# Kernel tuning notes

Measured on AMD Instinct MI355X. Metric: run time of the kernel, lower is better.

The kernel has to match this reference:

```python
import jax, jax.numpy as jnp
import numpy as np

D_MODEL = 1024
NUM_HEADS = 16
HEAD_DIM = D_MODEL // NUM_HEADS


def setup_inputs() -> dict:
    key = jax.random.key(0)
    ks = jax.random.split(key, 11)
    B, S, D = 2, 2048, D_MODEL
    s = 1.0 / np.sqrt(D)
    return {
        "query": jax.random.normal(ks[0], (B, S, D), jnp.float32),
        "key": jax.random.normal(ks[1], (B, S, D), jnp.float32),
        "value": jax.random.normal(ks[2], (B, S, D), jnp.float32),
        "w_q": jax.random.normal(ks[3], (D, D), jnp.float32) * s,
        "b_q": jnp.zeros((D,), jnp.float32),
        "w_k": jax.random.normal(ks[4], (D, D), jnp.float32) * s,
        "b_k": jnp.zeros((D,), jnp.float32),
        "w_v": jax.random.normal(ks[5], (D, D), jnp.float32) * s,
        "b_v": jnp.zeros((D,), jnp.float32),
        "w_o": jax.random.normal(ks[6], (D, D), jnp.float32) * s,
        "b_o": jnp.zeros((D,), jnp.float32),
    }


def reference(query, key, value, w_q, b_q, w_k, b_k, w_v, b_v, w_o, b_o):
    B, S, D = query.shape
    H, Hd = NUM_HEADS, HEAD_DIM
    # Linear layers (torch convention: x @ W.T + b)
    Q = (query @ w_q.T + b_q).reshape(B, S, H, Hd).transpose(0, 2, 1, 3)  # [B,H,S,Hd]
    K = (key @ w_k.T + b_k).reshape(B, S, H, Hd).transpose(0, 2, 1, 3)
    V = (value @ w_v.T + b_v).reshape(B, S, H, Hd).transpose(0, 2, 1, 3)
    scale = jnp.float32(np.sqrt(Hd))
    scores = jnp.einsum("bhqd,bhkd->bhqk", Q, K) / scale  # [B,H,S,S]
    attn_weights = jax.nn.softmax(scores, axis=-1)
    # dropout is identity in eval mode
    out = jnp.einsum("bhqk,bhkd->bhqd", attn_weights, V)  # [B,H,S,Hd]
    out = out.transpose(0, 2, 1, 3).reshape(B, S, D)
    out = out @ w_o.T + b_o
    return out, attn_weights
```

## Files before the change

kernel.cpp:

```cpp
#include <hip/hip_runtime.h>
#include <hip/hip_bf16.h>
#include <stdint.h>
#include <math.h>

typedef __attribute__((ext_vector_type(8))) short bf16x8;
typedef __attribute__((ext_vector_type(4))) float f32x4;
typedef __attribute__((ext_vector_type(8))) unsigned short ushort8;
typedef __attribute__((ext_vector_type(4))) unsigned short ushort4v;

#define LDS_AS(p) ((__attribute__((address_space(3))) void*)(p))
#define GLB_AS(p) ((const __attribute__((address_space(1))) void*)(p))

#define EXP2F(x) __builtin_amdgcn_exp2f(x)

__device__ __forceinline__ unsigned short f2bf(float f) {
  uint32_t u = __builtin_bit_cast(uint32_t, f);
  u += 0x7FFFu + ((u >> 16) & 1u);
  return (unsigned short)(u >> 16);
}

__global__ __launch_bounds__(256) void cvt_all_kernel(
    const float* __restrict__ q, const float* __restrict__ k, const float* __restrict__ v,
    const float* __restrict__ wq, const float* __restrict__ wk,
    const float* __restrict__ wv, const float* __restrict__ wo,
    unsigned short* __restrict__ oq, unsigned short* __restrict__ ok, unsigned short* __restrict__ ov,
    unsigned short* __restrict__ owq, unsigned short* __restrict__ owk,
    unsigned short* __restrict__ owv, unsigned short* __restrict__ owo) {
  int i = blockIdx.x * 256 + threadIdx.x;
  const float* src; unsigned short* dst; int off;
  if (i < 1572864) {
    int tsel = i / 524288; off = i - tsel * 524288;
    src = (tsel == 0) ? q : (tsel == 1) ? k : v;
    dst = (tsel == 0) ? oq : (tsel == 1) ? ok : ov;
  } else {
    int j = i - 1572864; int tsel = j >> 17; off = j & 131071;
    src = (tsel == 0) ? wq : (tsel == 1) ? wk : (tsel == 2) ? wv : wo;
    dst = (tsel == 0) ? owq : (tsel == 1) ? owk : (tsel == 2) ? owv : owo;
  }
  const f32x4* p = (const f32x4*)src + (size_t)off * 2;
  f32x4 a = p[0], b = p[1];
  ushort8 r;
  r[0] = f2bf(a[0]); r[1] = f2bf(a[1]); r[2] = f2bf(a[2]); r[3] = f2bf(a[3]);
  r[4] = f2bf(b[0]); r[5] = f2bf(b[1]); r[6] = f2bf(b[2]); r[7] = f2bf(b[3]);
  *((ushort8*)dst + off) = r;
}

template <int MODE>
__device__ __forceinline__ void gemm_bt_body(const unsigned short* __restrict__ A,
                                             const unsigned short* __restrict__ W,
                                             const float* __restrict__ bias,
                                             void* __restrict__ Cout, int N, int K,
                                             int mtile, int ntile) {
  __shared__ unsigned short As[128 * 64];
  __shared__ unsigned short Bs[128 * 64];
  const int t = threadIdx.x;
  const int lane = t & 63, wid = t >> 6;
  const int grp = lane >> 4, lr = lane & 15;
  const int wm = wid >> 1, wn = wid & 1;
  f32x4 acc[4][4] = {};
  for (int kt = 0; kt < K; kt += 64) {
    __syncthreads();
#pragma unroll
    for (int i = 0; i < 4; ++i) {
      int off = (i * 256 + t) * 16;
      int row = off >> 7, u8 = (off >> 4) & 7;
      const unsigned short* sa = A + (size_t)(mtile + row) * K + kt + u8 * 8;
      __builtin_amdgcn_global_load_lds(GLB_AS(sa), LDS_AS((char*)As + off), 16, 0, 0);
      const unsigned short* sb = W + (size_t)(ntile + row) * K + kt + u8 * 8;
      __builtin_amdgcn_global_load_lds(GLB_AS(sb), LDS_AS((char*)Bs + off), 16, 0, 0);
    }
    __syncthreads();
#pragma unroll
    for (int kc = 0; kc < 2; ++kc) {
      bf16x8 af[4], bfr[4];
#pragma unroll
      for (int mf = 0; mf < 4; ++mf) {
        int row = wm * 64 + mf * 16 + lr;
        af[mf] = *(const bf16x8*)((const char*)As + row * 128 + kc * 64 + grp * 16);
      }
#pragma unroll
      for (int nf = 0; nf < 4; ++nf) {
        int row = wn * 64 + nf * 16 + lr;
        bfr[nf] = *(const bf16x8*)((const char*)Bs + row * 128 + kc * 64 + grp * 16);
      }
#pragma unroll
      for (int mf = 0; mf < 4; ++mf)
#pragma unroll
        for (int nf = 0; nf < 4; ++nf)
          acc[mf][nf] = __builtin_amdgcn_mfma_f32_16x16x32_bf16(af[mf], bfr[nf], acc[mf][nf], 0, 0, 0);
    }
  }
#pragma unroll
  for (int nf = 0; nf < 4; ++nf) {
    int gcol = ntile + wn * 64 + nf * 16 + lr;
    float bv = bias[gcol];
#pragma unroll
    for (int mf = 0; mf < 4; ++mf) {
      int grow0 = mtile + wm * 64 + mf * 16 + grp * 4;
      if (MODE == 2) {
        ushort4v cv;
#pragma unroll
        for (int j = 0; j < 4; ++j) cv[j] = f2bf(acc[mf][nf][j] + bv);
        int bh = ((grow0 >> 11) << 4) | (gcol >> 6);
        *(ushort4v*)((unsigned short*)Cout +
                     ((size_t)(bh * 64 + (gcol & 63))) * 2048 + (grow0 & 2047)) = cv;
      } else {
#pragma unroll
        for (int j = 0; j < 4; ++j) {
          float v = acc[mf][nf][j] + bv;
          if (MODE == 1) ((unsigned short*)Cout)[(size_t)(grow0 + j) * N + gcol] = f2bf(v);
          else           ((float*)Cout)[(size_t)(grow0 + j) * N + gcol] = v;
        }
      }
    }
  }
}

__device__ __forceinline__ void gemm_swz(int& mtile, int& ntile) {
  int d0 = blockIdx.y * 8 + blockIdx.x;
  int L = (d0 & 7) * 32 + (d0 >> 3);
  ntile = (L & 7) * 128;
  mtile = (L >> 3) * 128;
}

__global__ __launch_bounds__(256) void gemm_qkv_kernel(
    const unsigned short* Xq, const unsigned short* Xk, const unsigned short* Xv,
    const unsigned short* Wq, const unsigned short* Wk, const unsigned short* Wv,
    const float* bq, const float* bk, const float* bv,
    unsigned short* Cq, unsigned short* Ck, unsigned short* Vt) {
  int mtile, ntile; gemm_swz(mtile, ntile);
  int z = blockIdx.z;
  if (z == 2)      gemm_bt_body<2>(Xv, Wv, bv, Vt, 1024, 1024, mtile, ntile);
  else if (z == 1) gemm_bt_body<1>(Xk, Wk, bk, Ck, 1024, 1024, mtile, ntile);
  else             gemm_bt_body<1>(Xq, Wq, bq, Cq, 1024, 1024, mtile, ntile);
}

__global__ __launch_bounds__(256) void gemm_out_kernel(const unsigned short* ctx,
                                                       const unsigned short* Wo,
                                                       const float* bo, float* out) {
  int mtile, ntile; gemm_swz(mtile, ntile);
  gemm_bt_body<0>(ctx, Wo, bo, out, 1024, 1024, mtile, ntile);
}

__global__ __launch_bounds__(256) void attn_kernel(const unsigned short* __restrict__ Qb,
                                                   const unsigned short* __restrict__ Kb,
                                                   const unsigned short* __restrict__ Vt,
                                                   float* __restrict__ attn,
                                                   unsigned short* __restrict__ ctx) {
  __shared__ unsigned short QP[4096];
  __shared__ unsigned short Ks[2][4096];
  __shared__ unsigned short Vs[2][4096];
  const int t = threadIdx.x;
  const int lane = t & 63, wid = t >> 6;
  const int grp = lane >> 4, lr = lane & 15;
  const int d0 = blockIdx.y * 32 + blockIdx.x;
  const int L = (d0 & 7) * 128 + (d0 >> 3);
  const int bh = L >> 5, qt = L & 31;
  const int b = bh >> 4, h = bh & 15;
  const int qbase = qt * 64;
  const unsigned short* Qg = Qb + ((size_t)(b * 2048 + qbase) * 1024 + h * 64);
  const unsigned short* Kg = Kb + ((size_t)(b * 2048) * 1024 + h * 64);
  const unsigned short* Vg = Vt + (size_t)bh * 64 * 2048;

  auto stageK = [&](int kt, int bs) {
#pragma unroll
    for (int i = 0; i < 2; ++i) {
      int off = (i * 256 + t) * 16;
      int row = off >> 7, u = (off >> 4) & 7, us = u ^ (row & 7);
      __builtin_amdgcn_global_load_lds(
          GLB_AS((const char*)(Kg + (size_t)kt * 64 * 1024) + row * 2048 + us * 16),
          LDS_AS((char*)Ks[bs] + off), 16, 0, 0);
    }
  };
  auto stageV = [&](int kt, int bs) {
#pragma unroll
    for (int i = 0; i < 2; ++i) {
      int off = (i * 256 + t) * 16;
      int row = off >> 7, u = (off >> 4) & 7, us = u ^ (row & 7);
      __builtin_amdgcn_global_load_lds(
          GLB_AS((const char*)(Vg + kt * 64) + row * 4096 + us * 16),
          LDS_AS((char*)Vs[bs] + off), 16, 0, 0);
    }
  };

#pragma unroll
  for (int i = 0; i < 2; ++i) {
    int off = (i * 256 + t) * 16;
    int row = off >> 7, u = (off >> 4) & 7, us = u ^ (row & 7);
    __builtin_amdgcn_global_load_lds(GLB_AS((const char*)Qg + row * 2048 + us * 16),
                                     LDS_AS((char*)QP + off), 16, 0, 0);
  }
  stageK(0, 0);
  __syncthreads();
  bf16x8 qf[2];
#pragma unroll
  for (int kc = 0; kc < 2; ++kc) {
    int row = wid * 16 + lr, c2 = kc * 64 + grp * 16;
    qf[kc] = *(const bf16x8*)((const char*)QP + (((row << 7) | c2) ^ ((row & 7) << 4)));
  }

  const float C1 = 0.18033688011112042f;
  float lsum = 0.f;
  for (int kt = 0; kt < 32; ++kt) {
    if (kt < 31) stageK(kt + 1, (kt + 1) & 1);
    const char* Kc = (const char*)Ks[kt & 1];
    f32x4 sacc[4] = {};
#pragma unroll
    for (int kc = 0; kc < 2; ++kc)
#pragma unroll
      for (int mf = 0; mf < 4; ++mf) {
        int row = mf * 16 + lr, c2 = kc * 64 + grp * 16;
        bf16x8 kf = *(const bf16x8*)(Kc + (((row << 7) | c2) ^ ((row & 7) << 4)));
        sacc[mf] = __builtin_amdgcn_mfma_f32_16x16x32_bf16(kf, qf[kc], sacc[mf], 0, 0, 0);
      }
#pragma unroll
    for (int mf = 0; mf < 4; ++mf)
#pragma unroll
      for (int j = 0; j < 4; ++j)
        lsum += EXP2F(sacc[mf][j] * C1);
    __syncthreads();
  }
  lsum += __shfl_xor(lsum, 16);
  lsum += __shfl_xor(lsum, 32);
  const float nl2l = -log2f(lsum);

  f32x4 oacc[4] = {};
  unsigned short* Pw = &QP[wid * 1024];
  const int q4 = lane >> 4, kseg = lane & 15;
  float* abase = attn + ((size_t)bh * 2048 + qbase + wid * 16) * 2048 + kseg * 4;
  stageK(0, 0); stageV(0, 0);
  __syncthreads();
  for (int kt = 0; kt < 32; ++kt) {
    if (kt < 31) { stageK(kt + 1, (kt + 1) & 1); stageV(kt + 1, (kt + 1) & 1); }
    __builtin_amdgcn_sched_barrier(0);
    const int cur = kt & 1;
    const char* Kc = (const char*)Ks[cur];
    const char* Vc = (const char*)Vs[cur];
    f32x4 sacc[4] = {};
#pragma unroll
    for (int kc = 0; kc < 2; ++kc)
#pragma unroll
      for (int mf = 0; mf < 4; ++mf) {
        int row = mf * 16 + lr, c2 = kc * 64 + grp * 16;
        bf16x8 kf = *(const bf16x8*)(Kc + (((row << 7) | c2) ^ ((row & 7) << 4)));
        sacc[mf] = __builtin_amdgcn_mfma_f32_16x16x32_bf16(kf, qf[kc], sacc[mf], 0, 0, 0);
      }
#pragma unroll
    for (int mf = 0; mf < 4; ++mf) {
      f32x4 pv;
#pragma unroll
      for (int j = 0; j < 4; ++j) pv[j] = EXP2F(__builtin_fmaf(sacc[mf][j], C1, nl2l));
      ushort4v pb;
#pragma unroll
      for (int j = 0; j < 4; ++j) pb[j] = f2bf(pv[j]);
      int c2 = (mf * 16 + grp * 4) * 2;
      *(ushort4v*)((char*)Pw + (((lr << 7) | c2) ^ ((lr & 7) << 4))) = pb;
    }
#pragma unroll
    for (int kc = 0; kc < 2; ++kc) {
      int c2 = kc * 64 + grp * 16;
      bf16x8 pf = *(const bf16x8*)((const char*)Pw + (((lr << 7) | c2) ^ ((lr & 7) << 4)));
#pragma unroll
      for (int df = 0; df < 4; ++df) {
        int row = df * 16 + lr;
        bf16x8 vf = *(const bf16x8*)(Vc + (((row << 7) | c2) ^ ((row & 7) << 4)));
        oacc[df] = __builtin_amdgcn_mfma_f32_16x16x32_bf16(vf, pf, oacc[df], 0, 0, 0);
      }
    }
#pragma unroll
    for (int i = 0; i < 4; ++i) {
      int qrow = i * 4 + q4;
      ushort4v pb4 = *(const ushort4v*)((const char*)Pw +
                       (((qrow << 7) | (kseg * 8)) ^ ((qrow & 7) << 4)));
      f32x4 pf4;
#pragma unroll
      for (int j = 0; j < 4; ++j)
        pf4[j] = __builtin_bit_cast(float, (uint32_t)((uint32_t)(unsigned short)pb4[j] << 16));
      __builtin_nontemporal_store(pf4, (f32x4*)(abase + (size_t)qrow * 2048 + kt * 64));
    }
    asm volatile("s_waitcnt vmcnt(4) lgkmcnt(0)" ::: "memory");
    __builtin_amdgcn_sched_barrier(0);
    __builtin_amdgcn_s_barrier();
  }
  unsigned short* crow = ctx + ((size_t)(b * 2048 + qbase + wid * 16 + lr) * 1024 + h * 64);
#pragma unroll
  for (int df = 0; df < 4; ++df) {
    ushort4v cv;
#pragma unroll
    for (int j = 0; j < 4; ++j) cv[j] = f2bf(oacc[df][j]);
    *(ushort4v*)(crow + df * 16 + grp * 4) = cv;
  }
}

extern "C" void kernel_launch(void* const* d_in, const int* in_sizes, int n_in,
                              void* d_out, int out_size, void* d_ws, size_t ws_size,
                              hipStream_t stream) {
  const float* query = (const float*)d_in[0];
  const float* key   = (const float*)d_in[1];
  const float* value = (const float*)d_in[2];
  const float* w_q = (const float*)d_in[3];
  const float* b_q = (const float*)d_in[4];
  const float* w_k = (const float*)d_in[5];
  const float* b_k = (const float*)d_in[6];
  const float* w_v = (const float*)d_in[7];
  const float* b_v = (const float*)d_in[8];
  const float* w_o = (const float*)d_in[9];
  const float* b_o = (const float*)d_in[10];

  float* out  = (float*)d_out;
  float* attn = out + (size_t)2 * 2048 * 1024;

  unsigned short* ws = (unsigned short*)d_ws;
  unsigned short* Xq = ws;
  unsigned short* Xk = Xq + 4194304;
  unsigned short* Xv = Xk + 4194304;
  unsigned short* Wq = Xv + 4194304;
  unsigned short* Wk = Wq + 1048576;
  unsigned short* Wv = Wk + 1048576;
  unsigned short* Wo = Wv + 1048576;
  unsigned short* Qb = Wo + 1048576;
  unsigned short* Kb = Qb + 4194304;
  unsigned short* Vt = Kb + 4194304;
  unsigned short* ctx = Vt + 4194304;

  cvt_all_kernel<<<8192, 256, 0, stream>>>(query, key, value, w_q, w_k, w_v, w_o,
                                           Xq, Xk, Xv, Wq, Wk, Wv, Wo);
  gemm_qkv_kernel<<<dim3(8, 32, 3), 256, 0, stream>>>(Xq, Xk, Xv, Wq, Wk, Wv,
                                                      b_q, b_k, b_v, Qb, Kb, Vt);
  attn_kernel<<<dim3(32, 32), 256, 0, stream>>>(Qb, Kb, Vt, attn, ctx);
  gemm_out_kernel<<<dim3(8, 32), 256, 0, stream>>>(ctx, Wo, b_o, out);
}
```

Before: 232.6 us.

## Split attention into separate row-sum and PV kernels via global lse buffer

Moves the first pass, which computes softmax row sums without subtracting a max, out of the fused attention kernel into its own lightweight kernel that writes -log2(sum) per query row to a workspace buffer. The second kernel reads that value, stages the first K/V tiles earlier, and only does the probability write-out and PV pass. The smaller kernels should need fewer registers and less LDS each, which may raise occupancy. The cost is an extra launch, a second read of Q and K, and a small global round trip for the row statistics. The row sum is also split into four partial accumulators to shorten the dependency chain.

```diff
diff --git a/kernel.cpp b/kernel.cpp
--- a/kernel.cpp
+++ b/kernel.cpp
@@ -142,11 +142,83 @@
   gemm_bt_body<0>(ctx, Wo, bo, out, 1024, 1024, mtile, ntile);
 }
 
-__global__ __launch_bounds__(256) void attn_kernel(const unsigned short* __restrict__ Qb,
-                                                   const unsigned short* __restrict__ Kb,
-                                                   const unsigned short* __restrict__ Vt,
-                                                   float* __restrict__ attn,
-                                                   unsigned short* __restrict__ ctx) {
+__global__ __launch_bounds__(256) void attn_lsum_kernel(const unsigned short* __restrict__ Qb,
+                                                        const unsigned short* __restrict__ Kb,
+                                                        float* __restrict__ lbuf) {
+  __shared__ unsigned short Qs[4096];
+  __shared__ unsigned short Ks[2][4096];
+  const int t = threadIdx.x;
+  const int lane = t & 63, wid = t >> 6;
+  const int grp = lane >> 4, lr = lane & 15;
+  const int d0 = blockIdx.y * 32 + blockIdx.x;
+  const int L = (d0 & 7) * 128 + (d0 >> 3);
+  const int bh = L >> 5, qt = L & 31;
+  const int b = bh >> 4, h = bh & 15;
+  const int qbase = qt * 64;
+  const unsigned short* Qg = Qb + ((size_t)(b * 2048 + qbase) * 1024 + h * 64);
+  const unsigned short* Kg = Kb + ((size_t)(b * 2048) * 1024 + h * 64);
+
+  auto stageK = [&](int kt, int bs) {
+#pragma unroll
+    for (int i = 0; i < 2; ++i) {
+      int off = (i * 256 + t) * 16;
+      int row = off >> 7, u = (off >> 4) & 7, us = u ^ (row & 7);
+      __builtin_amdgcn_global_load_lds(
+          GLB_AS((const char*)(Kg + (size_t)kt * 64 * 1024) + row * 2048 + us * 16),
+          LDS_AS((char*)Ks[bs] + off), 16, 0, 0);
+    }
+  };
+
+#pragma unroll
+  for (int i = 0; i < 2; ++i) {
+    int off = (i * 256 + t) * 16;
+    int row = off >> 7, u = (off >> 4) & 7, us = u ^ (row & 7);
+    __builtin_amdgcn_global_load_lds(GLB_AS((const char*)Qg + row * 2048 + us * 16),
+                                     LDS_AS((char*)Qs + off), 16, 0, 0);
+  }
+  stageK(0, 0);
+  __syncthreads();
+  bf16x8 qf[2];
+#pragma unroll
+  for (int kc = 0; kc < 2; ++kc) {
+    int row = wid * 16 + lr, c2 = kc * 64 + grp * 16;
+    qf[kc] = *(const bf16x8*)((const char*)Qs + (((row << 7) | c2) ^ ((row & 7) << 4)));
+  }
+
+  const float C1 = 0.18033688011112042f;
+  float ls[4] = {0.f, 0.f, 0.f, 0.f};
+  for (int kt = 0; kt < 32; ++kt) {
+    if (kt < 31) stageK(kt + 1, (kt + 1) & 1);
+    const char* Kc = (const char*)Ks[kt & 1];
+    f32x4 sacc[4] = {};
+#pragma unroll
+    for (int kc = 0; kc < 2; ++kc)
+#pragma unroll
+      for (int mf = 0; mf < 4; ++mf) {
+        int row = mf * 16 + lr, c2 = kc * 64 + grp * 16;
+        bf16x8 kf = *(const bf16x8*)(Kc + (((row << 7) | c2) ^ ((row & 7) << 4)));
+        sacc[mf] = __builtin_amdgcn_mfma_f32_16x16x32_bf16(kf, qf[kc], sacc[mf], 0, 0, 0);
+      }
+#pragma unroll
+    for (int mf = 0; mf < 4; ++mf)
+#pragma unroll
+      for (int j = 0; j < 4; ++j)
+        ls[mf] += EXP2F(sacc[mf][j] * C1);
+    __syncthreads();
+  }
+  float lsum = (ls[0] + ls[1]) + (ls[2] + ls[3]);
+  lsum += __shfl_xor(lsum, 16);
+  lsum += __shfl_xor(lsum, 32);
+  if (lane < 16)
+    lbuf[(size_t)bh * 2048 + qbase + wid * 16 + lr] = -log2f(lsum);
+}
+
+__global__ __launch_bounds__(256) void attn_pv_kernel(const unsigned short* __restrict__ Qb,
+                                                      const unsigned short* __restrict__ Kb,
+                                                      const unsigned short* __restrict__ Vt,
+                                                      const float* __restrict__ lbuf,
+                                                      float* __restrict__ attn,
+                                                      unsigned short* __restrict__ ctx) {
   __shared__ unsigned short QP[4096];
   __shared__ unsigned short Ks[2][4096];
   __shared__ unsigned short Vs[2][4096];
@@ -190,7 +262,8 @@
     __builtin_amdgcn_global_load_lds(GLB_AS((const char*)Qg + row * 2048 + us * 16),
                                      LDS_AS((char*)QP + off), 16, 0, 0);
   }
-  stageK(0, 0);
+  stageK(0, 0); stageV(0, 0);
+  const float nl2l = lbuf[(size_t)bh * 2048 + qbase + wid * 16 + lr];
   __syncthreads();
   bf16x8 qf[2];
 #pragma unroll
@@ -200,36 +273,10 @@
   }
 
   const float C1 = 0.18033688011112042f;
-  float lsum = 0.f;
-  for (int kt = 0; kt < 32; ++kt) {
-    if (kt < 31) stageK(kt + 1, (kt + 1) & 1);
-    const char* Kc = (const char*)Ks[kt & 1];
-    f32x4 sacc[4] = {};
-#pragma unroll
-    for (int kc = 0; kc < 2; ++kc)
-#pragma unroll
-      for (int mf = 0; mf < 4; ++mf) {
-        int row = mf * 16 + lr, c2 = kc * 64 + grp * 16;
-        bf16x8 kf = *(const bf16x8*)(Kc + (((row << 7) | c2) ^ ((row & 7) << 4)));
-        sacc[mf] = __builtin_amdgcn_mfma_f32_16x16x32_bf16(kf, qf[kc], sacc[mf], 0, 0, 0);
-      }
-#pragma unroll
-    for (int mf = 0; mf < 4; ++mf)
-#pragma unroll
-      for (int j = 0; j < 4; ++j)
-        lsum += EXP2F(sacc[mf][j] * C1);
-    __syncthreads();
-  }
-  lsum += __shfl_xor(lsum, 16);
-  lsum += __shfl_xor(lsum, 32);
-  const float nl2l = -log2f(lsum);
-
   f32x4 oacc[4] = {};
   unsigned short* Pw = &QP[wid * 1024];
   const int q4 = lane >> 4, kseg = lane & 15;
   float* abase = attn + ((size_t)bh * 2048 + qbase + wid * 16) * 2048 + kseg * 4;
-  stageK(0, 0); stageV(0, 0);
-  __syncthreads();
   for (int kt = 0; kt < 32; ++kt) {
     if (kt < 31) { stageK(kt + 1, (kt + 1) & 1); stageV(kt + 1, (kt + 1) & 1); }
     __builtin_amdgcn_sched_barrier(0);
@@ -322,11 +369,13 @@
   unsigned short* Kb = Qb + 4194304;
   unsigned short* Vt = Kb + 4194304;
   unsigned short* ctx = Vt + 4194304;
+  float* lbuf = (float*)(ctx + 4194304);
 
   cvt_all_kernel<<<8192, 256, 0, stream>>>(query, key, value, w_q, w_k, w_v, w_o,
                                            Xq, Xk, Xv, Wq, Wk, Wv, Wo);
   gemm_qkv_kernel<<<dim3(8, 32, 3), 256, 0, stream>>>(Xq, Xk, Xv, Wq, Wk, Wv,
                                                       b_q, b_k, b_v, Qb, Kb, Vt);
-  attn_kernel<<<dim3(32, 32), 256, 0, stream>>>(Qb, Kb, Vt, attn, ctx);
+  attn_lsum_kernel<<<dim3(32, 32), 256, 0, stream>>>(Qb, Kb, lbuf);
+  attn_pv_kernel<<<dim3(32, 32), 256, 0, stream>>>(Qb, Kb, Vt, lbuf, attn, ctx);
   gemm_out_kernel<<<dim3(8, 32), 256, 0, stream>>>(ctx, Wo, b_o, out);
 }
```

Result: slower. 244.4 us (+5.1%).
